# Performance work log

Measured on AMD Instinct MI355X. Metric: run time of the kernel, lower is better.

The kernel has to match this reference:

```python
import jax, jax.numpy as jnp
import numpy as np

EMB = 128
HEADS = 8
B = 8
T = 2048


def setup_inputs() -> dict:
    key = jax.random.key(0)
    ks = jax.random.split(key, 6)
    x = jax.random.normal(ks[0], (B, T, EMB), dtype=jnp.float32)
    # torch Linear(emb, heads*emb, bias=False): store as (in, out) so y = x @ W
    scale = 1.0 / np.sqrt(EMB)
    Wq = jax.random.uniform(ks[1], (EMB, HEADS * EMB), jnp.float32, -scale, scale)
    Wk = jax.random.uniform(ks[2], (EMB, HEADS * EMB), jnp.float32, -scale, scale)
    Wv = jax.random.uniform(ks[3], (EMB, HEADS * EMB), jnp.float32, -scale, scale)
    so = 1.0 / np.sqrt(HEADS * EMB)
    Wo = jax.random.uniform(ks[4], (HEADS * EMB, EMB), jnp.float32, -so, so)
    bo = jax.random.uniform(ks[5], (EMB,), jnp.float32, -so, so)
    return {"x": x, "Wq": Wq, "Wk": Wk, "Wv": Wv, "Wo": Wo, "bo": bo}


def reference(x, Wq, Wk, Wv, Wo, bo):
    b, t, e = x.shape
    h = HEADS
    q = (x @ Wq).reshape(b, t, h, e)  # [b,t,h,e]
    k = (x @ Wk).reshape(b, t, h, e)
    v = (x @ Wv).reshape(b, t, h, e)
    # scores: [b,h,q,k], scaled by sqrt(e) (per-head dim == emb here)
    scores = jnp.einsum('bqhe,bkhe->bhqk', q, k) / jnp.sqrt(jnp.asarray(e, x.dtype))
    attn = jax.nn.softmax(scores, axis=-1)
    out = jnp.einsum('bhqk,bkhe->bqhe', attn, v).reshape(b, t, h * e)
    return out @ Wo + bo
```

## Files before the change

### kernel.cpp

```cpp
#include <hip/hip_runtime.h>

using bf16x8 = __attribute__((ext_vector_type(8))) short;
using f32x4  = __attribute__((ext_vector_type(4))) float;
using f32x16 = __attribute__((ext_vector_type(16))) float;

__device__ __forceinline__ ushort f2bf(float f) {
    union { float f; unsigned int u; } c; c.f = f;
    unsigned int u = c.u;
    u = (u + 0x7fffu + ((u >> 16) & 1u)) >> 16;
    return (ushort)u;
}

#if defined(__has_builtin)
#if __has_builtin(__builtin_amdgcn_cvt_pk_bf16_f32)
#define HAS_PK_BF16 1
#endif
#if __has_builtin(__builtin_amdgcn_permlane32_swap)
#define HAS_PL32 1
#endif
#endif
__device__ __forceinline__ unsigned int pkbf(float a, float b) {
#ifdef HAS_PK_BF16
    typedef __bf16 bf2 __attribute__((ext_vector_type(2)));
    union { bf2 v; unsigned int u; } cv;
    cv.v = __builtin_amdgcn_cvt_pk_bf16_f32(a, b);
    return cv.u;
#else
    return (unsigned int)f2bf(a) | ((unsigned int)f2bf(b) << 16);
#endif
}

__device__ __forceinline__ void pl32swap(unsigned &a, unsigned &b) {
#ifdef HAS_PL32
    typedef unsigned uint2v __attribute__((ext_vector_type(2)));
    uint2v r = __builtin_amdgcn_permlane32_swap(a, b, false, false);
    a = r.x; b = r.y;
#else
    asm volatile("v_permlane32_swap_b32 %0, %1" : "+v"(a), "+v"(b));
#endif
}

__device__ __forceinline__ void dma16(const ushort* g, ushort* l) {
    __builtin_amdgcn_global_load_lds(
        (const __attribute__((address_space(1))) unsigned int*)g,
        (__attribute__((address_space(3))) unsigned int*)l, 16, 0, 0);
}

constexpr int BB   = 8;
constexpr int HH   = 8;
constexpr int TT   = 2048;
constexpr int DD   = 128;
#define C2F (0.08838834764831845f * 1.4426950408889634f)

__global__ void prep_kernel(const float* __restrict__ x,
                            const float* __restrict__ Wq, const float* __restrict__ Wk,
                            const float* __restrict__ Wv, const float* __restrict__ Wo,
                            ushort* __restrict__ xb, ushort* __restrict__ WqkvT,
                            ushort* __restrict__ WoT) {
    int t = blockIdx.x * 256 + threadIdx.x;
    if (t < 524288) {
        float4 v = ((const float4*)x)[t];
        ushort4 o;
        o.x = f2bf(v.x); o.y = f2bf(v.y); o.z = f2bf(v.z); o.w = f2bf(v.w);
        ((ushort4*)xb)[t] = o;
    } else if (t < 524288 + 393216) {
        int i = t - 524288;
        int j = i >> 7, kk = i & 127;
        const float* W = (j < 1024) ? Wq : ((j < 2048) ? Wk : Wv);
        int jj = j & 1023;
        WqkvT[j * 128 + kk] = f2bf(W[kk * 1024 + jj]);
    } else {
        int i = t - 917504;
        int e = i >> 10, kk = i & 1023;
        WoT[e * 1024 + kk] = f2bf(Wo[kk * 128 + e]);
    }
}

__global__ __launch_bounds__(256, 2)
void qkv_gemm(const ushort* __restrict__ xb, const ushort* __restrict__ WqkvT,
              ushort* __restrict__ q, ushort* __restrict__ k, ushort* __restrict__ vt) {
    __shared__ ushort Al[128 * 136];
    __shared__ ushort Bl[128 * 136];
    const int tid = threadIdx.x;
    const int n0 = blockIdx.x * 128, m0 = blockIdx.y * 128;

    for (int s = tid; s < 2048; s += 256) {
        int row = s >> 4, oct = s & 15;
        *(uint4*)&Al[row * 136 + oct * 8] = *(const uint4*)&xb[m0 * 128 + s * 8];
        *(uint4*)&Bl[row * 136 + oct * 8] = *(const uint4*)&WqkvT[n0 * 128 + s * 8];
    }
    __syncthreads();

    const int w = tid >> 6, lane = tid & 63, l15 = lane & 15, g = lane >> 4;
    const int wm = (w & 1) * 64, wn = (w >> 1) * 64;
    f32x4 acc[4][4] = {};

#pragma unroll
    for (int ks = 0; ks < 4; ks++) {
        bf16x8 af[4], bfr[4];
#pragma unroll
        for (int mb = 0; mb < 4; mb++)
            af[mb] = *(const bf16x8*)&Al[(wm + mb * 16 + l15) * 136 + ks * 32 + g * 8];
#pragma unroll
        for (int nb = 0; nb < 4; nb++)
            bfr[nb] = *(const bf16x8*)&Bl[(wn + nb * 16 + l15) * 136 + ks * 32 + g * 8];
#pragma unroll
        for (int mb = 0; mb < 4; mb++)
#pragma unroll
            for (int nb = 0; nb < 4; nb++)
                acc[mb][nb] = __builtin_amdgcn_mfma_f32_16x16x32_bf16(af[mb], bfr[nb], acc[mb][nb], 0, 0, 0);
    }

    const int which = n0 >> 10;
    const int b = m0 >> 11;
    const int h = (n0 >> 7) & 7;
    const int bh = b * HH + h;
    if (which == 0) {
#pragma unroll
        for (int mb = 0; mb < 4; mb++)
#pragma unroll
            for (int nb = 0; nb < 4; nb++)
#pragma unroll
                for (int r = 0; r < 4; r++) {
                    int t = (m0 + wm + mb * 16 + g * 4 + r) & 2047;
                    int e = wn + nb * 16 + l15;
                    q[((size_t)bh * TT + t) * DD + e] = f2bf(acc[mb][nb][r] * C2F);
                }
    } else if (which == 1) {
#pragma unroll
        for (int mb = 0; mb < 4; mb++)
#pragma unroll
            for (int nb = 0; nb < 4; nb++)
#pragma unroll
                for (int r = 0; r < 4; r++) {
                    int t = (m0 + wm + mb * 16 + g * 4 + r) & 2047;
                    int e = wn + nb * 16 + l15;
                    int esw = ((((e >> 3) ^ (t & 7)) << 3) | (e & 7));
                    k[((size_t)bh * TT + t) * DD + esw] = f2bf(acc[mb][nb][r]);
                }
    } else {
        __syncthreads();
        ushort* Tl = Al;
#pragma unroll
        for (int mb = 0; mb < 4; mb++)
#pragma unroll
            for (int nb = 0; nb < 4; nb++)
#pragma unroll
                for (int r = 0; r < 4; r++)
                    Tl[(wn + nb * 16 + l15) * 136 + wm + mb * 16 + g * 4 + r] = f2bf(acc[mb][nb][r]);
        __syncthreads();
        const int c0 = (m0 & 2047) >> 5;
        for (int s = tid; s < 2048; s += 256) {
            int e = s >> 4, x = s & 15;
            int cl = x >> 2, pos = x & 3;
            int el = e & 15;
            int vsw = (el ^ (el >> 2)) & 3;
            int tsrc = cl * 32 + ((pos ^ vsw) * 8);
            uint4 val = *(const uint4*)&Tl[e * 136 + tsrc];
            *(uint4*)&vt[(size_t)(((bh * 64 + c0 + cl) * 128) + e) * 32 + pos * 8] = val;
        }
    }
}

__global__ __launch_bounds__(256, 3)
void attn_kernel(const ushort* __restrict__ q, const ushort* __restrict__ k,
                 const ushort* __restrict__ vt, ushort* __restrict__ ao) {
    __shared__ ushort Kl[3][32 * 128];
    __shared__ ushort Vl[3][128 * 32];

    const int idx = blockIdx.x;
    const int h = idx & 7, b = (idx >> 3) & 7, qt128 = idx >> 6;
    const int t0 = qt128 * 128;
    const int bh = b * HH + h;
    const ushort* qg  = q  + (size_t)bh * TT * DD;
    const ushort* kg  = k  + (size_t)bh * TT * DD;
    const ushort* vtg = vt + (size_t)bh * 64 * DD * 32;

    const int tid = threadIdx.x, w = tid >> 6, lane = tid & 63;
    const int l31 = lane & 31, hi = lane >> 5, l15 = lane & 15;
    const int swk = lane & 7;
    const int swv = (l15 ^ (l15 >> 2)) & 3;

    bf16x8 qf[8];
#pragma unroll
    for (int ks = 0; ks < 8; ks++)
        qf[ks] = *(const bf16x8*)&qg[(size_t)(t0 + w * 32 + l31) * DD + ks * 16 + hi * 8];

    const int seg = tid * 8;
#pragma unroll
    for (int pc = 0; pc < 2; pc++)
#pragma unroll
        for (int j = 0; j < 2; j++) {
            dma16(kg  + (size_t)pc * 4096 + seg + j * 2048, &Kl[pc][seg + j * 2048]);
            dma16(vtg + (size_t)pc * 4096 + seg + j * 2048, &Vl[pc][seg + j * 2048]);
        }

    f32x16 o[4] = {};
    float ls = 0.0f;

    int cur = 0, nxt = 2;
    for (int c = 0; c < 64; c++) {
        if (c < 63) asm volatile("s_waitcnt vmcnt(4)" ::: "memory");
        else        asm volatile("s_waitcnt vmcnt(0)" ::: "memory");
        __builtin_amdgcn_s_barrier();
        __builtin_amdgcn_sched_barrier(0);

        bf16x8 kf[8];
#pragma unroll
        for (int ks = 0; ks < 8; ks++)
            kf[ks] = *(const bf16x8*)&Kl[cur][l31 * 128 + (((ks * 2 + hi) ^ swk) * 8)];
        if (c < 62) {
            const ushort* kn = kg + (size_t)(c + 2) * 4096;
#pragma unroll
            for (int j = 0; j < 2; j++)
                dma16(kn + seg + j * 2048, &Kl[nxt][seg + j * 2048]);
        }
        __builtin_amdgcn_s_barrier();
        asm volatile("s_waitcnt lgkmcnt(0)" ::: "memory");
        __builtin_amdgcn_sched_barrier(0);
        f32x16 st = {};
        __builtin_amdgcn_s_setprio(1);
#pragma unroll
        for (int ks = 0; ks < 8; ks++)
            st = __builtin_amdgcn_mfma_f32_32x32x16_bf16(kf[ks], qf[ks], st, 0, 0, 0);
        __builtin_amdgcn_s_setprio(0);
        __builtin_amdgcn_s_barrier();

        float p[16];
#pragma unroll
        for (int r = 0; r < 16; r++) p[r] = __builtin_amdgcn_exp2f(st[r]);
        ls += (((p[0] + p[1]) + (p[2] + p[3])) + ((p[4] + p[5]) + (p[6] + p[7])))
            + (((p[8] + p[9]) + (p[10] + p[11])) + ((p[12] + p[13]) + (p[14] + p[15])));
        unsigned a0 = pkbf(p[0],  p[1]),  a1 = pkbf(p[2],  p[3]);
        unsigned a2 = pkbf(p[4],  p[5]),  a3 = pkbf(p[6],  p[7]);
        unsigned a4 = pkbf(p[8],  p[9]),  a5 = pkbf(p[10], p[11]);
        unsigned a6 = pkbf(p[12], p[13]), a7 = pkbf(p[14], p[15]);
        pl32swap(a0, a2); pl32swap(a1, a3);
        pl32swap(a4, a6); pl32swap(a5, a7);
        union { unsigned u[4]; bf16x8 v; } A, B;
        A.u[0] = a0; A.u[1] = a1; A.u[2] = a2; A.u[3] = a3;
        B.u[0] = a4; B.u[1] = a5; B.u[2] = a6; B.u[3] = a7;
        bf16x8 paA = A.v, paB = B.v;

        bf16x8 vb[8];
#pragma unroll
        for (int et = 0; et < 4; et++)
#pragma unroll
            for (int ks2 = 0; ks2 < 2; ks2++)
                vb[et * 2 + ks2] = *(const bf16x8*)&Vl[cur][(et * 32 + l31) * 32 + (((ks2 * 2 + hi) ^ swv) * 8)];
        if (c < 62) {
            const ushort* vn = vtg + (size_t)(c + 2) * 4096;
#pragma unroll
            for (int j = 0; j < 2; j++)
                dma16(vn + seg + j * 2048, &Vl[nxt][seg + j * 2048]);
        }
        __builtin_amdgcn_s_barrier();
        asm volatile("s_waitcnt lgkmcnt(0)" ::: "memory");
        __builtin_amdgcn_sched_barrier(0);
        __builtin_amdgcn_s_setprio(1);
#pragma unroll
        for (int et = 0; et < 4; et++) {
            o[et] = __builtin_amdgcn_mfma_f32_32x32x16_bf16(paA, vb[et * 2 + 0], o[et], 0, 0, 0);
            o[et] = __builtin_amdgcn_mfma_f32_32x32x16_bf16(paB, vb[et * 2 + 1], o[et], 0, 0, 0);
        }
        __builtin_amdgcn_s_setprio(0);

        cur = (cur == 2) ? 0 : cur + 1;
        nxt = (nxt == 2) ? 0 : nxt + 1;
    }

    float tot = ls + __shfl_xor(ls, 32);
    const size_t aobase = (size_t)(b * TT) * 1024 + h * 128;
#pragma unroll
    for (int r = 0; r < 16; r++) {
        int ql = (r & 3) + 8 * (r >> 2) + 4 * hi;
        float inv = 1.0f / __shfl(tot, ql, 64);
        int m = t0 + w * 32 + ql;
#pragma unroll
        for (int et = 0; et < 4; et++)
            ao[aobase + (size_t)m * 1024 + et * 32 + l31] = f2bf(o[et][r] * inv);
    }
}

__global__ __launch_bounds__(256, 2)
void outproj_gemm(const ushort* __restrict__ ao, const ushort* __restrict__ WoT,
                  const float* __restrict__ bo, float* __restrict__ out) {
    __shared__ ushort Al[64 * 72];
    __shared__ ushort Bl[64 * 72];
    const int tid = threadIdx.x;
    const int n0 = blockIdx.x * 64, m0 = blockIdx.y * 64;
    const int w = tid >> 6, lane = tid & 63, l15 = lane & 15, g = lane >> 4;
    const int wm = (w & 1) * 32, wn = (w >> 1) * 32;
    f32x4 acc[2][2] = {};

    for (int kc = 0; kc < 16; kc++) {
        int k0 = kc * 64;
        __syncthreads();
        for (int s = tid; s < 512; s += 256) {
            int row = s >> 3, oct = s & 7;
            *(uint4*)&Al[row * 72 + oct * 8] = *(const uint4*)&ao[(size_t)(m0 + row) * 1024 + k0 + oct * 8];
            *(uint4*)&Bl[row * 72 + oct * 8] = *(const uint4*)&WoT[(n0 + row) * 1024 + k0 + oct * 8];
        }
        __syncthreads();
#pragma unroll
        for (int ks = 0; ks < 2; ks++) {
            bf16x8 af[2], bfr[2];
#pragma unroll
            for (int mb = 0; mb < 2; mb++)
                af[mb] = *(const bf16x8*)&Al[(wm + mb * 16 + l15) * 72 + ks * 32 + g * 8];
#pragma unroll
            for (int nb = 0; nb < 2; nb++)
                bfr[nb] = *(const bf16x8*)&Bl[(wn + nb * 16 + l15) * 72 + ks * 32 + g * 8];
#pragma unroll
            for (int mb = 0; mb < 2; mb++)
#pragma unroll
                for (int nb = 0; nb < 2; nb++)
                    acc[mb][nb] = __builtin_amdgcn_mfma_f32_16x16x32_bf16(af[mb], bfr[nb], acc[mb][nb], 0, 0, 0);
        }
    }

#pragma unroll
    for (int mb = 0; mb < 2; mb++)
#pragma unroll
        for (int nb = 0; nb < 2; nb++) {
            int j = n0 + wn + nb * 16 + l15;
            float bias = bo[j];
#pragma unroll
            for (int r = 0; r < 4; r++) {
                int m = m0 + wm + mb * 16 + g * 4 + r;
                out[(size_t)m * 128 + j] = acc[mb][nb][r] + bias;
            }
        }
}

extern "C" void kernel_launch(void* const* d_in, const int* in_sizes, int n_in,
                              void* d_out, int out_size, void* d_ws, size_t ws_size,
                              hipStream_t stream) {
    const float* x  = (const float*)d_in[0];
    const float* Wq = (const float*)d_in[1];
    const float* Wk = (const float*)d_in[2];
    const float* Wv = (const float*)d_in[3];
    const float* Wo = (const float*)d_in[4];
    const float* bo = (const float*)d_in[5];
    float* out = (float*)d_out;

    char* ws = (char*)d_ws;
    ushort* xb    = (ushort*)(ws);
    ushort* WqkvT = (ushort*)(ws + 4194304);
    ushort* WoT   = (ushort*)(ws + 4980736);
    ushort* qb    = (ushort*)(ws + 5242880);
    ushort* kb    = (ushort*)(ws + 38797312);
    ushort* vtb   = (ushort*)(ws + 72351744);
    ushort* ao    = (ushort*)(ws + 105906176);

    prep_kernel<<<4096, 256, 0, stream>>>(x, Wq, Wk, Wv, Wo, xb, WqkvT, WoT);
    qkv_gemm<<<dim3(24, 128), 256, 0, stream>>>(xb, WqkvT, qb, kb, vtb);
    attn_kernel<<<1024, 256, 0, stream>>>(qb, kb, vtb, ao);
    outproj_gemm<<<dim3(2, 256), 256, 0, stream>>>(ao, WoT, bo, out);
}
```

Measured before the change: 267.7 us.

## Software-pipeline attention loop: overlap QK MFMA of next chunk with PV of previous

Restructures the attention main loop so that each iteration computes the QK^T scores for chunk c while doing the softmax and PV MFMAs for chunk c-1, interleaving the two MFMA streams. K and V loads are merged into one DMA block, V gets a 4-deep LDS ring, and two of the per-iteration barriers are removed. The aim is to hide the exp/pack latency and barrier stalls behind matrix work. In exchange it uses more LDS and registers, and occupancy drops from 3 to 2 blocks per CU.

Result: slower. 283.0 us (+5.7%).

```diff
diff --git a/kernel.cpp b/kernel.cpp
--- a/kernel.cpp
+++ b/kernel.cpp
@@ -162,11 +162,11 @@
     }
 }
 
-__global__ __launch_bounds__(256, 3)
+__global__ __launch_bounds__(256, 2)
 void attn_kernel(const ushort* __restrict__ q, const ushort* __restrict__ k,
                  const ushort* __restrict__ vt, ushort* __restrict__ ao) {
     __shared__ ushort Kl[3][32 * 128];
-    __shared__ ushort Vl[3][128 * 32];
+    __shared__ ushort Vl[4][128 * 32];
 
     const int idx = blockIdx.x;
     const int h = idx & 7, b = (idx >> 3) & 7, qt128 = idx >> 6;
@@ -196,36 +196,11 @@
         }
 
     f32x16 o[4] = {};
+    f32x16 st = {};
     float ls = 0.0f;
 
-    int cur = 0, nxt = 2;
-    for (int c = 0; c < 64; c++) {
-        if (c < 63) asm volatile("s_waitcnt vmcnt(4)" ::: "memory");
-        else        asm volatile("s_waitcnt vmcnt(0)" ::: "memory");
-        __builtin_amdgcn_s_barrier();
-        __builtin_amdgcn_sched_barrier(0);
-
-        bf16x8 kf[8];
-#pragma unroll
-        for (int ks = 0; ks < 8; ks++)
-            kf[ks] = *(const bf16x8*)&Kl[cur][l31 * 128 + (((ks * 2 + hi) ^ swk) * 8)];
-        if (c < 62) {
-            const ushort* kn = kg + (size_t)(c + 2) * 4096;
-#pragma unroll
-            for (int j = 0; j < 2; j++)
-                dma16(kn + seg + j * 2048, &Kl[nxt][seg + j * 2048]);
-        }
-        __builtin_amdgcn_s_barrier();
-        asm volatile("s_waitcnt lgkmcnt(0)" ::: "memory");
-        __builtin_amdgcn_sched_barrier(0);
-        f32x16 st = {};
-        __builtin_amdgcn_s_setprio(1);
-#pragma unroll
-        for (int ks = 0; ks < 8; ks++)
-            st = __builtin_amdgcn_mfma_f32_32x32x16_bf16(kf[ks], qf[ks], st, 0, 0, 0);
-        __builtin_amdgcn_s_setprio(0);
-        __builtin_amdgcn_s_barrier();
-
+    bf16x8 paA, paB;
+    auto softmax_pa = [&]() {
         float p[16];
 #pragma unroll
         for (int r = 0; r < 16; r++) p[r] = __builtin_amdgcn_exp2f(st[r]);
@@ -240,33 +215,75 @@
         union { unsigned u[4]; bf16x8 v; } A, B;
         A.u[0] = a0; A.u[1] = a1; A.u[2] = a2; A.u[3] = a3;
         B.u[0] = a4; B.u[1] = a5; B.u[2] = a6; B.u[3] = a7;
-        bf16x8 paA = A.v, paB = B.v;
-
+        paA = A.v; paB = B.v;
+    };
+
+    for (int c = 0; c < 64; c++) {
+        if (c < 63) asm volatile("s_waitcnt vmcnt(4)" ::: "memory");
+        else        asm volatile("s_waitcnt vmcnt(0)" ::: "memory");
+        __builtin_amdgcn_s_barrier();
+        __builtin_amdgcn_sched_barrier(0);
+
+        bf16x8 kf[8];
+#pragma unroll
+        for (int ks = 0; ks < 8; ks++)
+            kf[ks] = *(const bf16x8*)&Kl[c % 3][l31 * 128 + (((ks * 2 + hi) ^ swk) * 8)];
         bf16x8 vb[8];
-#pragma unroll
-        for (int et = 0; et < 4; et++)
-#pragma unroll
-            for (int ks2 = 0; ks2 < 2; ks2++)
-                vb[et * 2 + ks2] = *(const bf16x8*)&Vl[cur][(et * 32 + l31) * 32 + (((ks2 * 2 + hi) ^ swv) * 8)];
+        if (c > 0) {
+#pragma unroll
+            for (int et = 0; et < 4; et++)
+#pragma unroll
+                for (int ks2 = 0; ks2 < 2; ks2++)
+                    vb[et * 2 + ks2] = *(const bf16x8*)&Vl[(c + 3) & 3][(et * 32 + l31) * 32 + (((ks2 * 2 + hi) ^ swv) * 8)];
+        }
+
         if (c < 62) {
+            const ushort* kn = kg  + (size_t)(c + 2) * 4096;
             const ushort* vn = vtg + (size_t)(c + 2) * 4096;
 #pragma unroll
-            for (int j = 0; j < 2; j++)
-                dma16(vn + seg + j * 2048, &Vl[nxt][seg + j * 2048]);
-        }
-        __builtin_amdgcn_s_barrier();
+            for (int j = 0; j < 2; j++) {
+                dma16(kn + seg + j * 2048, &Kl[(c + 2) % 3][seg + j * 2048]);
+                dma16(vn + seg + j * 2048, &Vl[(c + 2) & 3][seg + j * 2048]);
+            }
+        }
+
+        if (c > 0) softmax_pa();
+
         asm volatile("s_waitcnt lgkmcnt(0)" ::: "memory");
         __builtin_amdgcn_sched_barrier(0);
+
+        f32x16 stn = {};
         __builtin_amdgcn_s_setprio(1);
-#pragma unroll
-        for (int et = 0; et < 4; et++) {
-            o[et] = __builtin_amdgcn_mfma_f32_32x32x16_bf16(paA, vb[et * 2 + 0], o[et], 0, 0, 0);
-            o[et] = __builtin_amdgcn_mfma_f32_32x32x16_bf16(paB, vb[et * 2 + 1], o[et], 0, 0, 0);
+        if (c > 0) {
+#pragma unroll
+            for (int i = 0; i < 8; i++) {
+                stn = __builtin_amdgcn_mfma_f32_32x32x16_bf16(kf[i], qf[i], stn, 0, 0, 0);
+                o[i >> 1] = __builtin_amdgcn_mfma_f32_32x32x16_bf16(
+                    (i & 1) ? paB : paA, vb[i], o[i >> 1], 0, 0, 0);
+            }
+        } else {
+#pragma unroll
+            for (int i = 0; i < 8; i++)
+                stn = __builtin_amdgcn_mfma_f32_32x32x16_bf16(kf[i], qf[i], stn, 0, 0, 0);
         }
         __builtin_amdgcn_s_setprio(0);
-
-        cur = (cur == 2) ? 0 : cur + 1;
-        nxt = (nxt == 2) ? 0 : nxt + 1;
+        st = stn;
+    }
+
+    {
+        bf16x8 vb[8];
+#pragma unroll
+        for (int et = 0; et < 4; et++)
+#pragma unroll
+            for (int ks2 = 0; ks2 < 2; ks2++)
+                vb[et * 2 + ks2] = *(const bf16x8*)&Vl[3][(et * 32 + l31) * 32 + (((ks2 * 2 + hi) ^ swv) * 8)];
+        softmax_pa();
+        asm volatile("s_waitcnt lgkmcnt(0)" ::: "memory");
+        __builtin_amdgcn_sched_barrier(0);
+#pragma unroll
+        for (int i = 0; i < 8; i++)
+            o[i >> 1] = __builtin_amdgcn_mfma_f32_32x32x16_bf16(
+                (i & 1) ? paB : paA, vb[i], o[i >> 1], 0, 0, 0);
     }
 
     float tot = ls + __shfl_xor(ls, 32);
```

## Process two query tiles per wave in attention to reuse K/V fragments

Applied to the files above, without the earlier changes.

Each attention block now covers 256 queries instead of 128, with every wave holding two 32-row query tiles. Each K and V fragment read from LDS and each DMA'd chunk is reused across both tiles, which halves LDS traffic and global K/V loads per query and halves the grid. K and V loads are split into halves to limit register pressure. The cost is more registers (occupancy bound lowered from 3 to 2 blocks), and 512 blocks may fill the GPU less evenly.

Result: slower. 318.7 us (+19.1%).

```diff
diff --git a/kernel.cpp b/kernel.cpp
--- a/kernel.cpp
+++ b/kernel.cpp
@@ -162,15 +162,15 @@
     }
 }
 
-__global__ __launch_bounds__(256, 3)
+__global__ __launch_bounds__(256, 2)
 void attn_kernel(const ushort* __restrict__ q, const ushort* __restrict__ k,
                  const ushort* __restrict__ vt, ushort* __restrict__ ao) {
     __shared__ ushort Kl[3][32 * 128];
     __shared__ ushort Vl[3][128 * 32];
 
     const int idx = blockIdx.x;
-    const int h = idx & 7, b = (idx >> 3) & 7, qt128 = idx >> 6;
-    const int t0 = qt128 * 128;
+    const int h = idx & 7, b = (idx >> 3) & 7, qt256 = idx >> 6;
+    const int t0 = qt256 * 256;
     const int bh = b * HH + h;
     const ushort* qg  = q  + (size_t)bh * TT * DD;
     const ushort* kg  = k  + (size_t)bh * TT * DD;
@@ -181,10 +181,12 @@
     const int swk = lane & 7;
     const int swv = (l15 ^ (l15 >> 2)) & 3;
 
-    bf16x8 qf[8];
-#pragma unroll
-    for (int ks = 0; ks < 8; ks++)
-        qf[ks] = *(const bf16x8*)&qg[(size_t)(t0 + w * 32 + l31) * DD + ks * 16 + hi * 8];
+    bf16x8 qf[2][8];
+#pragma unroll
+    for (int qt = 0; qt < 2; qt++)
+#pragma unroll
+        for (int ks = 0; ks < 8; ks++)
+            qf[qt][ks] = *(const bf16x8*)&qg[(size_t)(t0 + w * 64 + qt * 32 + l31) * DD + ks * 16 + hi * 8];
 
     const int seg = tid * 8;
 #pragma unroll
@@ -195,8 +197,8 @@
             dma16(vtg + (size_t)pc * 4096 + seg + j * 2048, &Vl[pc][seg + j * 2048]);
         }
 
-    f32x16 o[4] = {};
-    float ls = 0.0f;
+    f32x16 o[2][4] = {};
+    float ls0 = 0.0f, ls1 = 0.0f;
 
     int cur = 0, nxt = 2;
     for (int c = 0; c < 64; c++) {
@@ -205,80 +207,143 @@
         __builtin_amdgcn_s_barrier();
         __builtin_amdgcn_sched_barrier(0);
 
-        bf16x8 kf[8];
-#pragma unroll
-        for (int ks = 0; ks < 8; ks++)
-            kf[ks] = *(const bf16x8*)&Kl[cur][l31 * 128 + (((ks * 2 + hi) ^ swk) * 8)];
-        if (c < 62) {
-            const ushort* kn = kg + (size_t)(c + 2) * 4096;
-#pragma unroll
-            for (int j = 0; j < 2; j++)
-                dma16(kn + seg + j * 2048, &Kl[nxt][seg + j * 2048]);
+        f32x16 st0 = {}, st1 = {};
+        {
+            bf16x8 kf[4];
+#pragma unroll
+            for (int ks = 0; ks < 4; ks++)
+                kf[ks] = *(const bf16x8*)&Kl[cur][l31 * 128 + (((ks * 2 + hi) ^ swk) * 8)];
+            if (c < 62) {
+                const ushort* kn = kg + (size_t)(c + 2) * 4096;
+#pragma unroll
+                for (int j = 0; j < 2; j++)
+                    dma16(kn + seg + j * 2048, &Kl[nxt][seg + j * 2048]);
+            }
+            __builtin_amdgcn_s_barrier();
+            asm volatile("s_waitcnt lgkmcnt(0)" ::: "memory");
+            __builtin_amdgcn_sched_barrier(0);
+            __builtin_amdgcn_s_setprio(1);
+#pragma unroll
+            for (int ks = 0; ks < 4; ks++) {
+                st0 = __builtin_amdgcn_mfma_f32_32x32x16_bf16(kf[ks], qf[0][ks], st0, 0, 0, 0);
+                st1 = __builtin_amdgcn_mfma_f32_32x32x16_bf16(kf[ks], qf[1][ks], st1, 0, 0, 0);
+            }
+            __builtin_amdgcn_s_setprio(0);
+        }
+        {
+            bf16x8 kf[4];
+#pragma unroll
+            for (int ks = 0; ks < 4; ks++)
+                kf[ks] = *(const bf16x8*)&Kl[cur][l31 * 128 + ((((ks + 4) * 2 + hi) ^ swk) * 8)];
+            __builtin_amdgcn_s_setprio(1);
+#pragma unroll
+            for (int ks = 0; ks < 4; ks++) {
+                st0 = __builtin_amdgcn_mfma_f32_32x32x16_bf16(kf[ks], qf[0][ks + 4], st0, 0, 0, 0);
+                st1 = __builtin_amdgcn_mfma_f32_32x32x16_bf16(kf[ks], qf[1][ks + 4], st1, 0, 0, 0);
+            }
+            __builtin_amdgcn_s_setprio(0);
         }
         __builtin_amdgcn_s_barrier();
-        asm volatile("s_waitcnt lgkmcnt(0)" ::: "memory");
-        __builtin_amdgcn_sched_barrier(0);
-        f32x16 st = {};
-        __builtin_amdgcn_s_setprio(1);
-#pragma unroll
-        for (int ks = 0; ks < 8; ks++)
-            st = __builtin_amdgcn_mfma_f32_32x32x16_bf16(kf[ks], qf[ks], st, 0, 0, 0);
-        __builtin_amdgcn_s_setprio(0);
-        __builtin_amdgcn_s_barrier();
-
-        float p[16];
-#pragma unroll
-        for (int r = 0; r < 16; r++) p[r] = __builtin_amdgcn_exp2f(st[r]);
-        ls += (((p[0] + p[1]) + (p[2] + p[3])) + ((p[4] + p[5]) + (p[6] + p[7])))
-            + (((p[8] + p[9]) + (p[10] + p[11])) + ((p[12] + p[13]) + (p[14] + p[15])));
-        unsigned a0 = pkbf(p[0],  p[1]),  a1 = pkbf(p[2],  p[3]);
-        unsigned a2 = pkbf(p[4],  p[5]),  a3 = pkbf(p[6],  p[7]);
-        unsigned a4 = pkbf(p[8],  p[9]),  a5 = pkbf(p[10], p[11]);
-        unsigned a6 = pkbf(p[12], p[13]), a7 = pkbf(p[14], p[15]);
-        pl32swap(a0, a2); pl32swap(a1, a3);
-        pl32swap(a4, a6); pl32swap(a5, a7);
-        union { unsigned u[4]; bf16x8 v; } A, B;
-        A.u[0] = a0; A.u[1] = a1; A.u[2] = a2; A.u[3] = a3;
-        B.u[0] = a4; B.u[1] = a5; B.u[2] = a6; B.u[3] = a7;
-        bf16x8 paA = A.v, paB = B.v;
-
-        bf16x8 vb[8];
-#pragma unroll
-        for (int et = 0; et < 4; et++)
-#pragma unroll
-            for (int ks2 = 0; ks2 < 2; ks2++)
-                vb[et * 2 + ks2] = *(const bf16x8*)&Vl[cur][(et * 32 + l31) * 32 + (((ks2 * 2 + hi) ^ swv) * 8)];
-        if (c < 62) {
-            const ushort* vn = vtg + (size_t)(c + 2) * 4096;
-#pragma unroll
-            for (int j = 0; j < 2; j++)
-                dma16(vn + seg + j * 2048, &Vl[nxt][seg + j * 2048]);
-        }
-        __builtin_amdgcn_s_barrier();
-        asm volatile("s_waitcnt lgkmcnt(0)" ::: "memory");
-        __builtin_amdgcn_sched_barrier(0);
-        __builtin_amdgcn_s_setprio(1);
-#pragma unroll
-        for (int et = 0; et < 4; et++) {
-            o[et] = __builtin_amdgcn_mfma_f32_32x32x16_bf16(paA, vb[et * 2 + 0], o[et], 0, 0, 0);
-            o[et] = __builtin_amdgcn_mfma_f32_32x32x16_bf16(paB, vb[et * 2 + 1], o[et], 0, 0, 0);
-        }
-        __builtin_amdgcn_s_setprio(0);
+
+        bf16x8 paA, paB, pbA, pbB;
+        {
+            float p[16];
+#pragma unroll
+            for (int r = 0; r < 16; r++) p[r] = __builtin_amdgcn_exp2f(st0[r]);
+            ls0 += (((p[0] + p[1]) + (p[2] + p[3])) + ((p[4] + p[5]) + (p[6] + p[7])))
+                 + (((p[8] + p[9]) + (p[10] + p[11])) + ((p[12] + p[13]) + (p[14] + p[15])));
+            unsigned a0 = pkbf(p[0],  p[1]),  a1 = pkbf(p[2],  p[3]);
+            unsigned a2 = pkbf(p[4],  p[5]),  a3 = pkbf(p[6],  p[7]);
+            unsigned a4 = pkbf(p[8],  p[9]),  a5 = pkbf(p[10], p[11]);
+            unsigned a6 = pkbf(p[12], p[13]), a7 = pkbf(p[14], p[15]);
+            pl32swap(a0, a2); pl32swap(a1, a3);
+            pl32swap(a4, a6); pl32swap(a5, a7);
+            union { unsigned u[4]; bf16x8 v; } A, B;
+            A.u[0] = a0; A.u[1] = a1; A.u[2] = a2; A.u[3] = a3;
+            B.u[0] = a4; B.u[1] = a5; B.u[2] = a6; B.u[3] = a7;
+            paA = A.v; paB = B.v;
+        }
+        {
+            float p[16];
+#pragma unroll
+            for (int r = 0; r < 16; r++) p[r] = __builtin_amdgcn_exp2f(st1[r]);
+            ls1 += (((p[0] + p[1]) + (p[2] + p[3])) + ((p[4] + p[5]) + (p[6] + p[7])))
+                 + (((p[8] + p[9]) + (p[10] + p[11])) + ((p[12] + p[13]) + (p[14] + p[15])));
+            unsigned a0 = pkbf(p[0],  p[1]),  a1 = pkbf(p[2],  p[3]);
+            unsigned a2 = pkbf(p[4],  p[5]),  a3 = pkbf(p[6],  p[7]);
+            unsigned a4 = pkbf(p[8],  p[9]),  a5 = pkbf(p[10], p[11]);
+            unsigned a6 = pkbf(p[12], p[13]), a7 = pkbf(p[14], p[15]);
+            pl32swap(a0, a2); pl32swap(a1, a3);
+            pl32swap(a4, a6); pl32swap(a5, a7);
+            union { unsigned u[4]; bf16x8 v; } A, B;
+            A.u[0] = a0; A.u[1] = a1; A.u[2] = a2; A.u[3] = a3;
+            B.u[0] = a4; B.u[1] = a5; B.u[2] = a6; B.u[3] = a7;
+            pbA = A.v; pbB = B.v;
+        }
+
+        {
+            bf16x8 vb[4];
+#pragma unroll
+            for (int u = 0; u < 4; u++) {
+                int et = u >> 1, ks2 = u & 1;
+                vb[u] = *(const bf16x8*)&Vl[cur][(et * 32 + l31) * 32 + (((ks2 * 2 + hi) ^ swv) * 8)];
+            }
+            if (c < 62) {
+                const ushort* vn = vtg + (size_t)(c + 2) * 4096;
+#pragma unroll
+                for (int j = 0; j < 2; j++)
+                    dma16(vn + seg + j * 2048, &Vl[nxt][seg + j * 2048]);
+            }
+            __builtin_amdgcn_s_barrier();
+            asm volatile("s_waitcnt lgkmcnt(0)" ::: "memory");
+            __builtin_amdgcn_sched_barrier(0);
+            __builtin_amdgcn_s_setprio(1);
+#pragma unroll
+            for (int et = 0; et < 2; et++) {
+                o[0][et] = __builtin_amdgcn_mfma_f32_32x32x16_bf16(paA, vb[et * 2 + 0], o[0][et], 0, 0, 0);
+                o[1][et] = __builtin_amdgcn_mfma_f32_32x32x16_bf16(pbA, vb[et * 2 + 0], o[1][et], 0, 0, 0);
+                o[0][et] = __builtin_amdgcn_mfma_f32_32x32x16_bf16(paB, vb[et * 2 + 1], o[0][et], 0, 0, 0);
+                o[1][et] = __builtin_amdgcn_mfma_f32_32x32x16_bf16(pbB, vb[et * 2 + 1], o[1][et], 0, 0, 0);
+            }
+            __builtin_amdgcn_s_setprio(0);
+        }
+        {
+            bf16x8 vb[4];
+#pragma unroll
+            for (int u = 0; u < 4; u++) {
+                int et = 2 + (u >> 1), ks2 = u & 1;
+                vb[u] = *(const bf16x8*)&Vl[cur][(et * 32 + l31) * 32 + (((ks2 * 2 + hi) ^ swv) * 8)];
+            }
+            __builtin_amdgcn_s_setprio(1);
+#pragma unroll
+            for (int eu = 0; eu < 2; eu++) {
+                int et = 2 + eu;
+                o[0][et] = __builtin_amdgcn_mfma_f32_32x32x16_bf16(paA, vb[eu * 2 + 0], o[0][et], 0, 0, 0);
+                o[1][et] = __builtin_amdgcn_mfma_f32_32x32x16_bf16(pbA, vb[eu * 2 + 0], o[1][et], 0, 0, 0);
+                o[0][et] = __builtin_amdgcn_mfma_f32_32x32x16_bf16(paB, vb[eu * 2 + 1], o[0][et], 0, 0, 0);
+                o[1][et] = __builtin_amdgcn_mfma_f32_32x32x16_bf16(pbB, vb[eu * 2 + 1], o[1][et], 0, 0, 0);
+            }
+            __builtin_amdgcn_s_setprio(0);
+        }
 
         cur = (cur == 2) ? 0 : cur + 1;
         nxt = (nxt == 2) ? 0 : nxt + 1;
     }
 
-    float tot = ls + __shfl_xor(ls, 32);
     const size_t aobase = (size_t)(b * TT) * 1024 + h * 128;
 #pragma unroll
-    for (int r = 0; r < 16; r++) {
-        int ql = (r & 3) + 8 * (r >> 2) + 4 * hi;
-        float inv = 1.0f / __shfl(tot, ql, 64);
-        int m = t0 + w * 32 + ql;
-#pragma unroll
-        for (int et = 0; et < 4; et++)
-            ao[aobase + (size_t)m * 1024 + et * 32 + l31] = f2bf(o[et][r] * inv);
+    for (int qt = 0; qt < 2; qt++) {
+        float lsq = qt ? ls1 : ls0;
+        float tot = lsq + __shfl_xor(lsq, 32);
+#pragma unroll
+        for (int r = 0; r < 16; r++) {
+            int ql = (r & 3) + 8 * (r >> 2) + 4 * hi;
+            float inv = 1.0f / __shfl(tot, ql, 64);
+            int m = t0 + w * 64 + qt * 32 + ql;
+#pragma unroll
+            for (int et = 0; et < 4; et++)
+                ao[aobase + (size_t)m * 1024 + et * 32 + l31] = f2bf(o[qt][et][r] * inv);
+        }
     }
 }
 
@@ -355,6 +420,6 @@
 
     prep_kernel<<<4096, 256, 0, stream>>>(x, Wq, Wk, Wv, Wo, xb, WqkvT, WoT);
     qkv_gemm<<<dim3(24, 128), 256, 0, stream>>>(xb, WqkvT, qb, kb, vtb);
-    attn_kernel<<<1024, 256, 0, stream>>>(qb, kb, vtb, ao);
+    attn_kernel<<<512, 256, 0, stream>>>(qb, kb, vtb, ao);
     outproj_gemm<<<dim3(2, 256), 256, 0, stream>>>(ao, WoT, bo, out);
 }
```
